# Performance work log

Hardware: AMD Instinct MI355X
Metric: run time of the kernel (lower is better)

## Reference

```python
import jax, jax.numpy as jnp
import numpy as np

# HOG config (matches init_kwargs / skimage defaults for block_norm='L2-Hys')
ORIENTATIONS = 9
CELL = 8          # pixels_per_cell (square)
BLOCK = 2         # cells_per_block (square)
EPS = 1e-5        # skimage block-norm epsilon


def setup_inputs() -> dict:
    key = jax.random.key(0)
    x = jax.random.uniform(key, (64, 1, 512, 512), dtype=jnp.float32)
    return {"x": x}


def _hog(img):
    # img: (B, H, W) grayscale float
    B, H, W = img.shape
    # skimage _hog_channel_gradient: central differences, zero at borders
    g_row = jnp.zeros_like(img).at[:, 1:-1, :].set(img[:, 2:, :] - img[:, :-2, :])
    g_col = jnp.zeros_like(img).at[:, :, 1:-1].set(img[:, :, 2:] - img[:, :, :-2])
    mag = jnp.hypot(g_row, g_col)
    # unsigned orientation in [0, 180)
    ori = jnp.degrees(jnp.arctan2(g_row, g_col)) % 180.0
    bin_width = 180.0 / ORIENTATIONS
    bin_idx = jnp.minimum((ori / bin_width).astype(jnp.int32), ORIENTATIONS - 1)

    ncr, ncc = H // CELL, W // CELL  # number of cells per row/col
    mag_c = mag[:, : ncr * CELL, : ncc * CELL].reshape(B, ncr, CELL, ncc, CELL)
    bin_c = bin_idx[:, : ncr * CELL, : ncc * CELL].reshape(B, ncr, CELL, ncc, CELL)

    # per-cell orientation histogram; skimage averages by cell area
    hists = []
    for i in range(ORIENTATIONS):  # small fixed loop over 9 bins
        hists.append(jnp.where(bin_c == i, mag_c, 0.0).sum(axis=(2, 4)))
    hist = jnp.stack(hists, axis=-1) / (CELL * CELL)  # (B, ncr, ncc, O)

    # sliding blocks of BLOCK x BLOCK cells, stride 1 cell
    nbr, nbc = ncr - BLOCK + 1, ncc - BLOCK + 1
    tmp = jnp.stack([hist[:, br : br + nbr] for br in range(BLOCK)], axis=2)       # (B,nbr,BLOCK,ncc,O)
    blocks = jnp.stack([tmp[:, :, :, bc : bc + nbc] for bc in range(BLOCK)], axis=4)  # (B,nbr,BLOCK,nbc,BLOCK,O)
    blocks = blocks.transpose(0, 1, 3, 2, 4, 5)  # (B, nbr, nbc, BLOCK, BLOCK, O)

    # L2-Hys normalization (skimage default block_norm)
    n1 = jnp.sqrt(jnp.sum(blocks * blocks, axis=(-3, -2, -1), keepdims=True) + EPS**2)
    b = jnp.minimum(blocks / n1, 0.2)
    n2 = jnp.sqrt(jnp.sum(b * b, axis=(-3, -2, -1), keepdims=True) + EPS**2)
    normalized = b / n2
    return normalized.reshape(B, -1)  # feature_vector=True ravel per image


def reference(x):
    return _hog(x[:, 0, :, :].astype(jnp.float32))
```

## Files before the change

kernel.cpp:

```cpp
#include <hip/hip_runtime.h>


#define ORIENT 9
#define IMH 512
#define IMW 512
#define NCR 64
#define NCC 64
#define NBR 63
#define NBC 63
#define NIMG 64

__global__ __launch_bounds__(256, 4) void hog_cell_hist(const float* __restrict__ img,
                                                        float* __restrict__ hist) {
    __shared__ float lh[32 * ORIENT];
    const int tx = threadIdx.x;
    const int ty = threadIdx.y;
    const int tid = ty * 32 + tx;

    lh[tid] = 0.f;
    if (tid < 32) lh[tid + 256] = 0.f;
    __syncthreads();

    const int c0 = blockIdx.x * 256 + tx * 8;
    const int r  = blockIdx.y * 8 + ty;
    const float* im = img + (size_t)blockIdx.z * (IMH * IMW) + (size_t)r * IMW + c0;

    const float4* imv = (const float4*)im;
    float4 a0 = imv[0], b0 = imv[1];
    float4 am = {0,0,0,0}, bm = {0,0,0,0};
    float4 ap = {0,0,0,0}, bp = {0,0,0,0};
    const bool rin = (r > 0) && (r < IMH - 1);
    if (r > 0)       { const float4* p = (const float4*)(im - IMW); am = p[0]; bm = p[1]; }
    if (r < IMH - 1) { const float4* p = (const float4*)(im + IMW); ap = p[0]; bp = p[1]; }
    const float left  = (c0 > 0)       ? im[-1] : 0.f;
    const float right = (c0 + 8 < IMW) ? im[8]  : 0.f;

    float rv[10] = {left, a0.x, a0.y, a0.z, a0.w, b0.x, b0.y, b0.z, b0.w, right};
    float pv[8]  = {ap.x, ap.y, ap.z, ap.w, bp.x, bp.y, bp.z, bp.w};
    float mv[8]  = {am.x, am.y, am.z, am.w, bm.x, bm.y, bm.z, bm.w};

    float mags[8];
    int   bins[8];
#pragma unroll
    for (int j = 0; j < 8; ++j) {
        const float gr = rin ? (pv[j] - mv[j]) : 0.f;
        const bool cin = (c0 + j > 0) && (c0 + j < IMW - 1);
        const float gc = cin ? (rv[j + 2] - rv[j]) : 0.f;
        mags[j] = sqrtf(gr * gr + gc * gc);
        float ori = atan2f(gr, gc) * 57.29577951308232f;
        ori = (ori >= 180.0f) ? ori - 180.0f : ori;
        ori = (ori <   0.0f) ? ori + 180.0f : ori;
        int bin = (int)(ori / 20.0f);
        bins[j] = bin > (ORIENT - 1) ? (ORIENT - 1) : bin;
    }
    float* cellh = &lh[tx * ORIENT];
#pragma unroll
    for (int j = 0; j < 8; ++j) atomicAdd(&cellh[bins[j]], mags[j]);
    __syncthreads();

    float* hrow = hist + (((size_t)blockIdx.z * NCR + blockIdx.y) * NCC + blockIdx.x * 32) * ORIENT;
    hrow[tid] = lh[tid] * (1.f / 64.f);
    if (tid < 32) hrow[tid + 256] = lh[tid + 256] * (1.f / 64.f);
}

__global__ __launch_bounds__(64) void hog_block_norm(const float* __restrict__ hist,
                                                     float* __restrict__ out) {
    __shared__ float lh[2 * NCC * ORIENT];
    const int tid = threadIdx.x;
    const int br  = blockIdx.x;
    const int b   = blockIdx.y;

    const float4* src = (const float4*)(hist + ((size_t)b * NCR + br) * (NCC * ORIENT));
    float4* dst = (float4*)lh;
#pragma unroll
    for (int k = 0; k < 5; ++k) {
        int idx = k * 64 + tid;
        if (idx < 288) dst[idx] = src[idx];
    }
    __syncthreads();

    const int bc = tid;
    if (bc >= NBC) return;

    float v[36];
    float s = 0.f;
#pragma unroll
    for (int k = 0; k < 18; ++k) { float h = lh[bc * ORIENT + k];               v[k]      = h; s += h * h; }
#pragma unroll
    for (int k = 0; k < 18; ++k) { float h = lh[NCC * ORIENT + bc * ORIENT + k]; v[18 + k] = h; s += h * h; }

    const float r1 = 1.0f / sqrtf(s + 1e-10f);
    float s2 = 0.f;
#pragma unroll
    for (int k = 0; k < 36; ++k) {
        float x = fminf(v[k] * r1, 0.2f);
        v[k] = x;
        s2 += x * x;
    }
    const float r2 = 1.0f / sqrtf(s2 + 1e-10f);

    float4* o = (float4*)(out + (((size_t)b * NBR + br) * NBC + bc) * 36);
#pragma unroll
    for (int k = 0; k < 9; ++k)
        o[k] = make_float4(v[4*k] * r2, v[4*k+1] * r2, v[4*k+2] * r2, v[4*k+3] * r2);
}

extern "C" void kernel_launch(void* const* d_in, const int* in_sizes, int n_in,
                              void* d_out, int out_size, void* d_ws, size_t ws_size,
                              hipStream_t stream) {
    const float* x = (const float*)d_in[0];
    float* out  = (float*)d_out;
    float* hist = (float*)d_ws;

    dim3 b1(32, 8, 1);
    dim3 g1(IMW / 256, IMH / 8, NIMG);
    hipLaunchKernelGGL(hog_cell_hist, g1, b1, 0, stream, x, hist);

    dim3 b2(64, 1, 1);
    dim3 g2(NBR, NIMG, 1);
    hipLaunchKernelGGL(hog_block_norm, g2, b2, 0, stream, hist, out);
}
```

Measured before the change: 195.0 us.

## Stage full-width row strips in LDS via direct global-to-LDS loads for cell histograms

```diff
diff --git a/kernel.cpp b/kernel.cpp
--- a/kernel.cpp
+++ b/kernel.cpp
@@ -10,57 +10,80 @@
 #define NBC 63
 #define NIMG 64
 
-__global__ __launch_bounds__(256, 4) void hog_cell_hist(const float* __restrict__ img,
-                                                        float* __restrict__ hist) {
-    __shared__ float lh[32 * ORIENT];
-    const int tx = threadIdx.x;
-    const int ty = threadIdx.y;
-    const int tid = ty * 32 + tx;
+#if defined(__has_builtin)
+#if __has_builtin(__builtin_amdgcn_sqrtf)
+#define FAST_SQRT(x) __builtin_amdgcn_sqrtf(x)
+#else
+#define FAST_SQRT(x) sqrtf(x)
+#endif
+#else
+#define FAST_SQRT(x) sqrtf(x)
+#endif
 
-    lh[tid] = 0.f;
-    if (tid < 32) lh[tid + 256] = 0.f;
+__global__ __launch_bounds__(512) void hog_cell_hist(const float* __restrict__ img,
+                                                     float* __restrict__ hist) {
+    __shared__ float lds[10 * IMW];
+    __shared__ float lh[NCC * ORIENT];
+    const int tid  = threadIdx.x;
+    const int lane = tid & 63;
+    const int wv   = tid >> 6;
+    const int strip = blockIdx.x;
+    const int b     = blockIdx.y;
+    const int rA    = strip * 8;
+    const float* im = img + (size_t)b * (IMH * IMW);
+
+    lh[tid % 576] = 0.f;
+    if (tid < 64) lh[512 + tid] = 0.f;
+
+    for (int k = wv; k < 20; k += 8) {
+        const int t = k >> 1, h = k & 1;
+        const int g = rA - 1 + t;
+        float* ldst = &lds[t * IMW + h * 256];
+        if ((unsigned)g < IMH) {
+            const float* gsrc = im + ((size_t)g * IMW + h * 256 + lane * 4);
+            __builtin_amdgcn_global_load_lds(
+                (const __attribute__((address_space(1))) void*)gsrc,
+                (__attribute__((address_space(3))) void*)ldst, 16, 0, 0);
+        } else {
+            float4 z = {0.f, 0.f, 0.f, 0.f};
+            *(float4*)(ldst + lane * 4) = z;
+        }
+    }
     __syncthreads();
 
-    const int c0 = blockIdx.x * 256 + tx * 8;
-    const int r  = blockIdx.y * 8 + ty;
-    const float* im = img + (size_t)blockIdx.z * (IMH * IMW) + (size_t)r * IMW + c0;
+    const int c = tid;
+    float col[10];
+#pragma unroll
+    for (int t = 0; t < 10; ++t) col[t] = lds[t * IMW + c];
+    const int cl = (c > 0)       ? c - 1 : 0;
+    const int cr = (c < IMW - 1) ? c + 1 : IMW - 1;
+    float lf[8], rg[8];
+#pragma unroll
+    for (int t = 0; t < 8; ++t) { lf[t] = lds[(t + 1) * IMW + cl]; rg[t] = lds[(t + 1) * IMW + cr]; }
 
-    const float4* imv = (const float4*)im;
-    float4 a0 = imv[0], b0 = imv[1];
-    float4 am = {0,0,0,0}, bm = {0,0,0,0};
-    float4 ap = {0,0,0,0}, bp = {0,0,0,0};
-    const bool rin = (r > 0) && (r < IMH - 1);
-    if (r > 0)       { const float4* p = (const float4*)(im - IMW); am = p[0]; bm = p[1]; }
-    if (r < IMH - 1) { const float4* p = (const float4*)(im + IMW); ap = p[0]; bp = p[1]; }
-    const float left  = (c0 > 0)       ? im[-1] : 0.f;
-    const float right = (c0 + 8 < IMW) ? im[8]  : 0.f;
-
-    float rv[10] = {left, a0.x, a0.y, a0.z, a0.w, b0.x, b0.y, b0.z, b0.w, right};
-    float pv[8]  = {ap.x, ap.y, ap.z, ap.w, bp.x, bp.y, bp.z, bp.w};
-    float mv[8]  = {am.x, am.y, am.z, am.w, bm.x, bm.y, bm.z, bm.w};
-
-    float mags[8];
-    int   bins[8];
+    const bool cin = (c > 0) && (c < IMW - 1);
+    float mags[8]; int bins[8];
 #pragma unroll
-    for (int j = 0; j < 8; ++j) {
-        const float gr = rin ? (pv[j] - mv[j]) : 0.f;
-        const bool cin = (c0 + j > 0) && (c0 + j < IMW - 1);
-        const float gc = cin ? (rv[j + 2] - rv[j]) : 0.f;
-        mags[j] = sqrtf(gr * gr + gc * gc);
+    for (int t = 0; t < 8; ++t) {
+        const int r = rA + t;
+        const bool rin = (r > 0) && (r < IMH - 1);
+        const float gr = rin ? (col[t + 2] - col[t]) : 0.f;
+        const float gc = cin ? (rg[t] - lf[t])       : 0.f;
+        mags[t] = FAST_SQRT(gr * gr + gc * gc);
         float ori = atan2f(gr, gc) * 57.29577951308232f;
         ori = (ori >= 180.0f) ? ori - 180.0f : ori;
         ori = (ori <   0.0f) ? ori + 180.0f : ori;
         int bin = (int)(ori / 20.0f);
-        bins[j] = bin > (ORIENT - 1) ? (ORIENT - 1) : bin;
+        bins[t] = bin > (ORIENT - 1) ? (ORIENT - 1) : bin;
     }
-    float* cellh = &lh[tx * ORIENT];
+    float* cellh = &lh[(c >> 3) * ORIENT];
 #pragma unroll
-    for (int j = 0; j < 8; ++j) atomicAdd(&cellh[bins[j]], mags[j]);
+    for (int t = 0; t < 8; ++t) atomicAdd(&cellh[bins[t]], mags[t]);
     __syncthreads();
 
-    float* hrow = hist + (((size_t)blockIdx.z * NCR + blockIdx.y) * NCC + blockIdx.x * 32) * ORIENT;
+    float* hrow = hist + (((size_t)b * NCR + strip) * NCC) * ORIENT;
     hrow[tid] = lh[tid] * (1.f / 64.f);
-    if (tid < 32) hrow[tid + 256] = lh[tid + 256] * (1.f / 64.f);
+    if (tid < 64) hrow[512 + tid] = lh[512 + tid] * (1.f / 64.f);
 }
 
 __global__ __launch_bounds__(64) void hog_block_norm(const float* __restrict__ hist,
@@ -85,7 +108,7 @@
     float v[36];
     float s = 0.f;
 #pragma unroll
-    for (int k = 0; k < 18; ++k) { float h = lh[bc * ORIENT + k];               v[k]      = h; s += h * h; }
+    for (int k = 0; k < 18; ++k) { float h = lh[bc * ORIENT + k];                v[k]      = h; s += h * h; }
 #pragma unroll
     for (int k = 0; k < 18; ++k) { float h = lh[NCC * ORIENT + bc * ORIENT + k]; v[18 + k] = h; s += h * h; }
 
@@ -112,8 +135,8 @@
     float* out  = (float*)d_out;
     float* hist = (float*)d_ws;
 
-    dim3 b1(32, 8, 1);
-    dim3 g1(IMW / 256, IMH / 8, NIMG);
+    dim3 b1(512, 1, 1);
+    dim3 g1(NCR, NIMG, 1);
     hipLaunchKernelGGL(hog_cell_hist, g1, b1, 0, stream, x, hist);
 
     dim3 b2(64, 1, 1);
```

Result: no change. 196.2 us (+0.6%).
